# Kernel tuning notes

Hardware: AMD Instinct MI355X
Metric: run time of the kernel (lower is better)

Reference implementation:

```python
import jax, jax.numpy as jnp
import numpy as np

B, S, D, H = 1, 2048, 2048, 16
HD = D // H  # head_dim = 128
EPS = 1e-6


def setup_inputs() -> dict:
    key = jax.random.key(0)
    ks = jax.random.split(key, 12)
    sc = 0.02
    x = jax.random.normal(ks[0], (B, S, D), jnp.float32)
    wq = jax.random.normal(ks[1], (D, D), jnp.float32) * sc
    bq = jnp.zeros((D,), jnp.float32)
    wk = jax.random.normal(ks[2], (D, D), jnp.float32) * sc
    bk = jnp.zeros((D,), jnp.float32)
    wv = jax.random.normal(ks[3], (D, D), jnp.float32) * sc
    bv = jnp.zeros((D,), jnp.float32)
    wo = jax.random.normal(ks[4], (D, D), jnp.float32) * sc
    bo = jnp.zeros((D,), jnp.float32)
    gq = jnp.ones((D,), jnp.float32)  # RMSNorm weight for q
    gk = jnp.ones((D,), jnp.float32)  # RMSNorm weight for k
    # Rotary frequency table: complex freqs = cos + i*sin, shape [S, 1, HD//2]
    pos = jnp.arange(S, dtype=jnp.float32)
    inv = 1.0 / (10000.0 ** (jnp.arange(0, HD, 2, dtype=jnp.float32) / HD))  # [HD//2]
    theta = pos[:, None] * inv[None, :]  # [S, HD//2]
    freqs_cos = jnp.cos(theta)[:, None, :]  # [S, 1, HD//2]
    freqs_sin = jnp.sin(theta)[:, None, :]
    return {"x": x, "wq": wq, "bq": bq, "wk": wk, "bk": bk, "wv": wv, "bv": bv,
            "wo": wo, "bo": bo, "gq": gq, "gk": gk,
            "freqs_cos": freqs_cos, "freqs_sin": freqs_sin}


def _rmsnorm(x, g):
    # RMSNorm over full model dim (applied BEFORE head split, as in source)
    return x * jax.lax.rsqrt(jnp.mean(x * x, axis=-1, keepdims=True) + EPS) * g


def _rope(x, cos, sin):
    # x: [B,S,D] -> (B,S,H,HD//2,2) complex pairs; complex mult by (cos + i sin)
    b, s, d = x.shape
    xr = x.reshape(b, s, H, HD // 2, 2)
    a, bb = xr[..., 0], xr[..., 1]
    # cos/sin [S,1,HD//2] broadcast against [B,S,H,HD//2]
    ra = a * cos - bb * sin
    rb = a * sin + bb * cos
    return jnp.stack([ra, rb], axis=-1).reshape(b, s, d)


def reference(x, wq, bq, wk, bk, wv, bv, wo, bo, gq, gk, freqs_cos, freqs_sin):
    b, s, d = x.shape
    q = _rope(_rmsnorm(x @ wq.T + bq, gq), freqs_cos, freqs_sin)
    k = _rope(_rmsnorm(x @ wk.T + bk, gk), freqs_cos, freqs_sin)
    v = x @ wv.T + bv
    qh = q.reshape(b, s, H, HD).transpose(0, 2, 1, 3)  # [B,H,S,HD]
    kh = k.reshape(b, s, H, HD).transpose(0, 2, 1, 3)
    vh = v.reshape(b, s, H, HD).transpose(0, 2, 1, 3)
    scores = jnp.einsum('bhqd,bhkd->bhqk', qh, kh) / np.sqrt(HD).astype(np.float32)
    attn = jax.nn.softmax(scores, axis=-1)
    out = jnp.einsum('bhqk,bhkd->bhqd', attn, vh)
    out = out.transpose(0, 2, 1, 3).reshape(b, s, d)
    return out @ wo.T + bo
```

## Files before the change

### kernel.cpp

```cpp
#include <hip/hip_runtime.h>
#include <math.h>

typedef unsigned short u16;
typedef unsigned int u32;
typedef __bf16 bf16x8 __attribute__((ext_vector_type(8)));
typedef float f32x4 __attribute__((ext_vector_type(4)));
typedef float f32x16 __attribute__((ext_vector_type(16)));

__device__ __forceinline__ u16 f2bf(float f) {
  unsigned u = __float_as_uint(f);
  u += 0x7fff + ((u >> 16) & 1);
  return (u16)(u >> 16);
}

__device__ __forceinline__ u32 cvtpk(float lo, float hi) {
  u32 r;
  asm("v_cvt_pk_bf16_f32 %0, %1, %2" : "=v"(r) : "v"(lo), "v"(hi));
  return r;
}

__device__ __forceinline__ void pswap(u32& x, u32& y) {
  asm volatile("v_permlane32_swap_b32 %0, %1" : "+v"(x), "+v"(y));
}

__device__ __forceinline__ void gload_lds16(const void* g, void* l) {
  __builtin_amdgcn_global_load_lds(
      (const __attribute__((address_space(1))) unsigned int*)g,
      (__attribute__((address_space(3))) unsigned int*)l, 16, 0, 0);
}

__global__ __launch_bounds__(256) void k_cvt5(const float* __restrict__ s0,
                                              const float* __restrict__ s1,
                                              const float* __restrict__ s2,
                                              const float* __restrict__ s3,
                                              const float* __restrict__ s4,
                                              u16* __restrict__ dx,
                                              u16* __restrict__ dqkv,
                                              u16* __restrict__ dwo) {
  const int y = blockIdx.y;
  const float* s = (y == 0) ? s0 : (y == 1) ? s1 : (y == 2) ? s2
                   : (y == 3) ? s3 : s4;
  u16* d = (y == 0) ? dx : (y == 4) ? dwo : dqkv + (size_t)(y - 1) * 4194304;
  int i = (blockIdx.x * 256 + threadIdx.x) * 4;
  float4 v = *(const float4*)(s + i);
  ushort4 o;
  o.x = f2bf(v.x); o.y = f2bf(v.y); o.z = f2bf(v.z); o.w = f2bf(v.w);
  *(ushort4*)(d + i) = o;
}

__global__ __launch_bounds__(512, 4) void k_gemm_big(const u16* __restrict__ A,
                                                     const u16* __restrict__ B,
                                                     float* __restrict__ C,
                                                     int M, int N, int K) {
  __shared__ __align__(16) char lds[2][40960];
  const int tid = threadIdx.x;
  const int wid = tid >> 6, lane = tid & 63;
  const int lr = lane & 15, lg = lane >> 4;
  const int wm = (wid >> 2) * 64, wn = (wid & 3) * 48;
  const int nbx = N / 192, nby = M >> 7;
  const int colsPerXcd = nbx >> 3;
  const int xcd = blockIdx.x & 7, idx = blockIdx.x >> 3;
  const int bx = xcd * colsPerXcd + idx / nby;
  const int by = idx % nby;
  const int bm = by * 128, bn = bx * 192;
  const int srow = tid >> 3;
  const int schunk = (tid & 7) ^ (srow & 7);
  const size_t rsK = (size_t)K * 2;
  const char* gA = (const char*)A + (size_t)(bm + srow) * rsK + schunk * 16;
  const char* gB = (const char*)B + (size_t)(bn + srow) * rsK + schunk * 16;
  char* dA = (char*)lds + wid * 1024;
  char* dB = (char*)lds + 16384 + wid * 1024;

#define STAGE(cur, k0)                                                         \
  {                                                                            \
    _Pragma("unroll") for (int i = 0; i < 2; ++i)                              \
        gload_lds16(gA + (size_t)(i * 64) * rsK + (size_t)(k0) * 2,            \
                    dA + (cur) * 40960 + i * 8192);                            \
    _Pragma("unroll") for (int i = 0; i < 3; ++i)                              \
        gload_lds16(gB + (size_t)(i * 64) * rsK + (size_t)(k0) * 2,            \
                    dB + (cur) * 40960 + i * 8192);                            \
  }

  f32x4 acc[4][3] = {};
  STAGE(0, 0);
  STAGE(1, 64);
  asm volatile("s_waitcnt vmcnt(5)" ::: "memory");
  __builtin_amdgcn_s_barrier();
  const int NT = K >> 6;
  int cur = 0;
  const int rsw = (lr & 7);
  for (int t = 0; t < NT; ++t) {
    const char* La = (const char*)lds + cur * 40960;
    const char* Lb = La + 16384;
    bf16x8 af[4][2], bfr[3][2];
#pragma unroll
    for (int mi = 0; mi < 4; ++mi)
#pragma unroll
      for (int kk = 0; kk < 2; ++kk)
        af[mi][kk] = *(const bf16x8*)(La + (wm + mi * 16 + lr) * 128 +
                                      (((kk * 4 + lg) ^ rsw) * 16));
#pragma unroll
    for (int ni = 0; ni < 3; ++ni)
#pragma unroll
      for (int kk = 0; kk < 2; ++kk)
        bfr[ni][kk] = *(const bf16x8*)(Lb + (wn + ni * 16 + lr) * 128 +
                                       (((kk * 4 + lg) ^ rsw) * 16));
    asm volatile("s_waitcnt lgkmcnt(0)" ::: "memory");
    __builtin_amdgcn_s_barrier();
    if (t + 2 < NT) STAGE(cur, (t + 2) << 6);
    __builtin_amdgcn_s_setprio(1);
#pragma unroll
    for (int kk = 0; kk < 2; ++kk)
#pragma unroll
      for (int mi = 0; mi < 4; ++mi)
#pragma unroll
        for (int ni = 0; ni < 3; ++ni)
          acc[mi][ni] = __builtin_amdgcn_mfma_f32_16x16x32_bf16(
              af[mi][kk], bfr[ni][kk], acc[mi][ni], 0, 0, 0);
    __builtin_amdgcn_s_setprio(0);
    if (t + 2 < NT)
      asm volatile("s_waitcnt vmcnt(5)" ::: "memory");
    else
      asm volatile("s_waitcnt vmcnt(0)" ::: "memory");
    __builtin_amdgcn_s_barrier();
    cur ^= 1;
  }
#undef STAGE
#pragma unroll
  for (int mi = 0; mi < 4; ++mi)
#pragma unroll
    for (int ni = 0; ni < 3; ++ni)
#pragma unroll
      for (int j = 0; j < 4; ++j)
        C[(size_t)(bm + wm + mi * 16 + lg * 4 + j) * N + bn + wn + ni * 16 + lr] =
            acc[mi][ni][j];
}

__global__ __launch_bounds__(256, 2) void k_gemm_pipe(const u16* __restrict__ A,
                                                      const u16* __restrict__ B,
                                                      const float* __restrict__ bias,
                                                      float* __restrict__ C,
                                                      int M, int N, int K) {
  __shared__ __align__(16) char lds[2][24576];
  const int tid = threadIdx.x;
  const int wid = tid >> 6, lane = tid & 63;
  const int lr = lane & 15, lg = lane >> 4;
  const int wm = (wid >> 1) * 64, wn = (wid & 1) * 32;
  const int nbx = N >> 6, nby = M >> 7;
  const int colsPerXcd = nbx >> 3;
  const int xcd = blockIdx.x & 7, idx = blockIdx.x >> 3;
  const int bx = xcd * colsPerXcd + idx / nby;
  const int by = idx % nby;
  const int bm = by * 128, bn = bx * 64;
  const int srow = tid >> 3;
  const int schunk = (tid & 7) ^ (srow & 7);
  const size_t rsK = (size_t)K * 2;
  const char* gA = (const char*)A + (size_t)(bm + srow) * rsK + schunk * 16;
  const char* gB = (const char*)B + (size_t)(bn + srow) * rsK + schunk * 16;
  char* dA = (char*)lds + wid * 1024;
  char* dB = (char*)lds + 16384 + wid * 1024;

#define STAGE(cur, k0)                                                         \
  {                                                                            \
    _Pragma("unroll") for (int i = 0; i < 4; ++i)                              \
        gload_lds16(gA + (size_t)(i * 32) * rsK + (size_t)(k0) * 2,            \
                    dA + (cur) * 24576 + i * 4096);                            \
    _Pragma("unroll") for (int i = 0; i < 2; ++i)                              \
        gload_lds16(gB + (size_t)(i * 32) * rsK + (size_t)(k0) * 2,            \
                    dB + (cur) * 24576 + i * 4096);                            \
  }

  f32x4 acc[4][2] = {};
  STAGE(0, 0);
  STAGE(1, 64);
  asm volatile("s_waitcnt vmcnt(6)" ::: "memory");
  __builtin_amdgcn_s_barrier();
  const int NT = K >> 6;
  int cur = 0;
  const int rsw = (lr & 7);
  for (int t = 0; t < NT; ++t) {
    const char* La = (const char*)lds + cur * 24576;
    const char* Lb = La + 16384;
    bf16x8 af[4][2], bfr[2][2];
#pragma unroll
    for (int mi = 0; mi < 4; ++mi)
#pragma unroll
      for (int kk = 0; kk < 2; ++kk)
        af[mi][kk] = *(const bf16x8*)(La + (wm + mi * 16 + lr) * 128 +
                                      (((kk * 4 + lg) ^ rsw) * 16));
#pragma unroll
    for (int ni = 0; ni < 2; ++ni)
#pragma unroll
      for (int kk = 0; kk < 2; ++kk)
        bfr[ni][kk] = *(const bf16x8*)(Lb + (wn + ni * 16 + lr) * 128 +
                                       (((kk * 4 + lg) ^ rsw) * 16));
    asm volatile("s_waitcnt lgkmcnt(0)" ::: "memory");
    __builtin_amdgcn_s_barrier();
    if (t + 2 < NT) STAGE(cur, (t + 2) << 6);
    __builtin_amdgcn_s_setprio(1);
#pragma unroll
    for (int kk = 0; kk < 2; ++kk)
#pragma unroll
      for (int mi = 0; mi < 4; ++mi)
#pragma unroll
        for (int ni = 0; ni < 2; ++ni)
          acc[mi][ni] = __builtin_amdgcn_mfma_f32_16x16x32_bf16(
              af[mi][kk], bfr[ni][kk], acc[mi][ni], 0, 0, 0);
    __builtin_amdgcn_s_setprio(0);
    if (t + 2 < NT)
      asm volatile("s_waitcnt vmcnt(6)" ::: "memory");
    else
      asm volatile("s_waitcnt vmcnt(0)" ::: "memory");
    __builtin_amdgcn_s_barrier();
    cur ^= 1;
  }
#undef STAGE
#pragma unroll
  for (int mi = 0; mi < 4; ++mi)
#pragma unroll
    for (int ni = 0; ni < 2; ++ni) {
      int col = bn + wn + ni * 16 + lr;
      float bb = bias[col];
#pragma unroll
      for (int j = 0; j < 4; ++j)
        C[(size_t)(bm + wm + mi * 16 + lg * 4 + j) * N + col] =
            acc[mi][ni][j] + bb;
    }
}

__global__ __launch_bounds__(256) void k_rmsnorm_rope(
    const float* __restrict__ qkv, const float* __restrict__ bq,
    const float* __restrict__ bk, const float* __restrict__ gq,
    const float* __restrict__ gk, const float* __restrict__ fcos,
    const float* __restrict__ fsin, u16* __restrict__ qb, u16* __restrict__ kb) {
  const int s = blockIdx.x, which = blockIdx.y;
  const int t = threadIdx.x;
  const float* src = qkv + (size_t)s * 6144 + which * 2048;
  const float* bias = which ? bk : bq;
  const float* g = which ? gk : gq;
  u16* dst = (which ? kb : qb) + (size_t)s * 2048;
  const int c0 = t * 8;
  float4 a0 = *(const float4*)(src + c0);
  float4 a1 = *(const float4*)(src + c0 + 4);
  float4 b0 = *(const float4*)(bias + c0);
  float4 b1 = *(const float4*)(bias + c0 + 4);
  float v[8];
  v[0] = a0.x + b0.x; v[1] = a0.y + b0.y; v[2] = a0.z + b0.z; v[3] = a0.w + b0.w;
  v[4] = a1.x + b1.x; v[5] = a1.y + b1.y; v[6] = a1.z + b1.z; v[7] = a1.w + b1.w;
  float ss = 0.f;
#pragma unroll
  for (int j = 0; j < 8; ++j) ss += v[j] * v[j];
#pragma unroll
  for (int m = 1; m < 64; m <<= 1) ss += __shfl_xor(ss, m);
  __shared__ float red[4];
  if ((t & 63) == 0) red[t >> 6] = ss;
  __syncthreads();
  float r = rsqrtf((red[0] + red[1] + red[2] + red[3]) * (1.0f / 2048.0f) + 1e-6f);
  if (!which) r *= 0.08838834764831843f * 1.4426950408889634f;
  float4 g0 = *(const float4*)(g + c0);
  float4 g1 = *(const float4*)(g + c0 + 4);
  float gg[8] = {g0.x, g0.y, g0.z, g0.w, g1.x, g1.y, g1.z, g1.w};
  const int p0 = (c0 & 127) >> 1;
  u16 o[8];
#pragma unroll
  for (int j = 0; j < 4; ++j) {
    float a = v[2 * j] * r * gg[2 * j];
    float b = v[2 * j + 1] * r * gg[2 * j + 1];
    float co = fcos[s * 64 + p0 + j], si = fsin[s * 64 + p0 + j];
    o[2 * j]     = f2bf(a * co - b * si);
    o[2 * j + 1] = f2bf(a * si + b * co);
  }
  ushort4 q0; q0.x = o[0]; q0.y = o[1]; q0.z = o[2]; q0.w = o[3];
  ushort4 q1; q1.x = o[4]; q1.y = o[5]; q1.z = o[6]; q1.w = o[7];
  *(ushort4*)(dst + c0) = q0;
  *(ushort4*)(dst + c0 + 4) = q1;
}

__global__ __launch_bounds__(256) void k_transpose_v(const float* __restrict__ qkv,
                                                     const float* __restrict__ bv,
                                                     u16* __restrict__ vT) {
  __shared__ float tile[64][65];
  const int s0 = blockIdx.x * 64, d0 = blockIdx.y * 64;
  const int t = threadIdx.x;
  const int tc = (t & 15) * 4, tr = t >> 4;
  float4 bb = *(const float4*)(bv + d0 + tc);
#pragma unroll
  for (int i = 0; i < 4; ++i) {
    int sr = tr + i * 16;
    float4 x = *(const float4*)(qkv + (size_t)(s0 + sr) * 6144 + 4096 + d0 + tc);
    tile[sr][tc + 0] = x.x + bb.x;
    tile[sr][tc + 1] = x.y + bb.y;
    tile[sr][tc + 2] = x.z + bb.z;
    tile[sr][tc + 3] = x.w + bb.w;
  }
  __syncthreads();
#pragma unroll
  for (int i = 0; i < 4; ++i) {
    int dr = tr + i * 16;
    ushort4 o;
    o.x = f2bf(tile[tc + 0][dr]);
    o.y = f2bf(tile[tc + 1][dr]);
    o.z = f2bf(tile[tc + 2][dr]);
    o.w = f2bf(tile[tc + 3][dr]);
    *(ushort4*)(vT + (size_t)(d0 + dr) * 2048 + s0 + tc) = o;
  }
}

__global__ __launch_bounds__(256, 2) void k_attn(const u16* __restrict__ qb,
                                                 const u16* __restrict__ kb,
                                                 const u16* __restrict__ vT,
                                                 float* __restrict__ opart,
                                                 float* __restrict__ ml) {
  __shared__ __align__(16) char Ks[2][16384];
  __shared__ __align__(16) char Vs[2][16384];
  const int qt = blockIdx.x, h = blockIdx.y, ks = blockIdx.z;
  const int tid = threadIdx.x;
  const int wid = tid >> 6, lane = tid & 63;
  const int l31 = lane & 31, hi = lane >> 5;
  const int q0w = qt * 128 + wid * 32;
  const char* kbB = (const char*)kb;
  const char* vTB = (const char*)vT;
  const int krow = tid >> 4;
  const int kc = (tid & 15) ^ krow;
  const int vrow = tid >> 3;
  const int vc = (tid & 7) ^ (vrow & 7);

#define STAGE(buf, k0)                                                         \
  {                                                                            \
    _Pragma("unroll") for (int i = 0; i < 4; ++i)                              \
        gload_lds16(kbB + (size_t)((k0) + i * 16 + krow) * 4096 + h * 256 +    \
                        kc * 16,                                               \
                    (char*)Ks + (buf) * 16384 + i * 4096 + wid * 1024);        \
    _Pragma("unroll") for (int i = 0; i < 4; ++i)                              \
        gload_lds16(vTB + (size_t)(h * 128 + i * 32 + vrow) * 4096 +           \
                        (size_t)(k0) * 2 + vc * 16,                            \
                    (char*)Vs + (buf) * 16384 + i * 4096 + wid * 1024);        \
  }

  bf16x8 qf[8];
#pragma unroll
  for (int ds = 0; ds < 8; ++ds)
    qf[ds] = *(const bf16x8*)(qb + (size_t)(q0w + l31) * 2048 + h * 128 +
                              ds * 16 + hi * 8);
  f32x16 o[4] = {};
  float mrun = -3.0e38f, lsum = 0.f;
  const int kbeg = ks * 1024;
  const int ksw = l31 & 15, vsw = l31 & 7;
  STAGE(0, kbeg);
  __syncthreads();
  int cur = 0;
  for (int t = 0; t < 16; ++t) {
    if (t + 1 < 16) STAGE(cur ^ 1, kbeg + (t + 1) * 64);
    const char* Kc = Ks[cur];
    const char* Vc = Vs[cur];
    f32x16 p0 = {}, p1 = {};
    __builtin_amdgcn_s_setprio(1);
#pragma unroll
    for (int ds = 0; ds < 8; ++ds) {
      bf16x8 kf0 = *(const bf16x8*)(Kc + l31 * 256 + (((ds * 2 + hi) ^ ksw) * 16));
      p0 = __builtin_amdgcn_mfma_f32_32x32x16_bf16(kf0, qf[ds], p0, 0, 0, 0);
      bf16x8 kf1 = *(const bf16x8*)(Kc + (32 + l31) * 256 +
                                    (((ds * 2 + hi) ^ ksw) * 16));
      p1 = __builtin_amdgcn_mfma_f32_32x32x16_bf16(kf1, qf[ds], p1, 0, 0, 0);
    }
    __builtin_amdgcn_s_setprio(0);
    float pm = p0[0];
#pragma unroll
    for (int r = 1; r < 16; ++r) pm = fmaxf(pm, p0[r]);
#pragma unroll
    for (int r = 0; r < 16; ++r) pm = fmaxf(pm, p1[r]);
    pm = fmaxf(pm, __shfl_xor(pm, 32));
    if (!__all(pm <= mrun + 8.0f)) {
      float nm = fmaxf(mrun, pm);
      float fv = __builtin_amdgcn_exp2f(mrun - nm);
#pragma unroll
      for (int dt = 0; dt < 4; ++dt) o[dt] *= fv;
      lsum *= fv;
      mrun = nm;
    }
    float ls = 0.f;
#pragma unroll
    for (int r = 0; r < 16; ++r) { p0[r] = __builtin_amdgcn_exp2f(p0[r] - mrun); ls += p0[r]; }
#pragma unroll
    for (int r = 0; r < 16; ++r) { p1[r] = __builtin_amdgcn_exp2f(p1[r] - mrun); ls += p1[r]; }
    ls += __shfl_xor(ls, 32);
    lsum += ls;
    bf16x8 pa[4];
#pragma unroll
    for (int sl = 0; sl < 2; ++sl) {
      u32 E0 = cvtpk(p0[8 * sl + 0], p0[8 * sl + 1]);
      u32 E1 = cvtpk(p0[8 * sl + 2], p0[8 * sl + 3]);
      u32 O0 = cvtpk(p0[8 * sl + 4], p0[8 * sl + 5]);
      u32 O1 = cvtpk(p0[8 * sl + 6], p0[8 * sl + 7]);
      pswap(E0, O0); pswap(E1, O1);
      union { u32 w[4]; bf16x8 v; } uu;
      uu.w[0] = E0; uu.w[1] = E1; uu.w[2] = O0; uu.w[3] = O1;
      pa[sl] = uu.v;
    }
#pragma unroll
    for (int sl = 0; sl < 2; ++sl) {
      u32 E0 = cvtpk(p1[8 * sl + 0], p1[8 * sl + 1]);
      u32 E1 = cvtpk(p1[8 * sl + 2], p1[8 * sl + 3]);
      u32 O0 = cvtpk(p1[8 * sl + 4], p1[8 * sl + 5]);
      u32 O1 = cvtpk(p1[8 * sl + 6], p1[8 * sl + 7]);
      pswap(E0, O0); pswap(E1, O1);
      union { u32 w[4]; bf16x8 v; } uu;
      uu.w[0] = E0; uu.w[1] = E1; uu.w[2] = O0; uu.w[3] = O1;
      pa[2 + sl] = uu.v;
    }
    __builtin_amdgcn_s_setprio(1);
#pragma unroll
    for (int s = 0; s < 4; ++s)
#pragma unroll
      for (int dt = 0; dt < 4; ++dt) {
        bf16x8 vf = *(const bf16x8*)(Vc + (dt * 32 + l31) * 128 +
                                     (((s * 2 + hi) ^ vsw) * 16));
        o[dt] = __builtin_amdgcn_mfma_f32_32x32x16_bf16(pa[s], vf, o[dt], 0, 0, 0);
      }
    __builtin_amdgcn_s_setprio(0);
    __syncthreads();
    cur ^= 1;
  }
#undef STAGE
  float* opb = opart + ((size_t)ks * 32768 + (size_t)h * 2048 + q0w) * 128 + l31;
#pragma unroll
  for (int dt = 0; dt < 4; ++dt)
#pragma unroll
    for (int r = 0; r < 16; ++r)
      opb[(size_t)((r & 3) + 8 * (r >> 2) + 4 * hi) * 128 + dt * 32] = o[dt][r];
  if (lane < 32) {
    float2 v2; v2.x = mrun; v2.y = lsum;
    *(float2*)(ml + ((size_t)ks * 32768 + (size_t)h * 2048 + q0w + l31) * 2) = v2;
  }
}

__global__ __launch_bounds__(256) void k_attn_merge(const float* __restrict__ opart,
                                                    const float* __restrict__ ml,
                                                    u16* __restrict__ ob) {
  const int r = blockIdx.x * 8 + (threadIdx.x >> 5);
  const int d0 = (threadIdx.x & 31) * 4;
  float2 ml0 = *(const float2*)(ml + (size_t)r * 2);
  float2 ml1 = *(const float2*)(ml + (size_t)(32768 + r) * 2);
  float M = fmaxf(ml0.x, ml1.x);
  float f0 = __builtin_amdgcn_exp2f(ml0.x - M);
  float f1 = __builtin_amdgcn_exp2f(ml1.x - M);
  float inv = 1.0f / (ml0.y * f0 + ml1.y * f1);
  float4 a = *(const float4*)(opart + (size_t)r * 128 + d0);
  float4 b = *(const float4*)(opart + (size_t)(32768 + r) * 128 + d0);
  int h = r >> 11, q = r & 2047;
  ushort4 o;
  o.x = f2bf((a.x * f0 + b.x * f1) * inv);
  o.y = f2bf((a.y * f0 + b.y * f1) * inv);
  o.z = f2bf((a.z * f0 + b.z * f1) * inv);
  o.w = f2bf((a.w * f0 + b.w * f1) * inv);
  *(ushort4*)(ob + (size_t)q * 2048 + h * 128 + d0) = o;
}

extern "C" void kernel_launch(void* const* d_in, const int* in_sizes, int n_in,
                              void* d_out, int out_size, void* d_ws, size_t ws_size,
                              hipStream_t stream) {
  const float* x    = (const float*)d_in[0];
  const float* wq   = (const float*)d_in[1];
  const float* bq   = (const float*)d_in[2];
  const float* wk   = (const float*)d_in[3];
  const float* bk   = (const float*)d_in[4];
  const float* wv   = (const float*)d_in[5];
  const float* bv   = (const float*)d_in[6];
  const float* wo   = (const float*)d_in[7];
  const float* bo   = (const float*)d_in[8];
  const float* gq   = (const float*)d_in[9];
  const float* gk   = (const float*)d_in[10];
  const float* fcos = (const float*)d_in[11];
  const float* fsin = (const float*)d_in[12];

  char* ws = (char*)d_ws;
  float* qkv_pre = (float*)ws;
  float* opart = (float*)ws;
  float* ml    = (float*)(ws + 33554432);
  u16* xb   = (u16*)(ws + 50331648);
  u16* wqkv = (u16*)(ws + 58720256);
  u16* qb   = (u16*)(ws + 50331648);
  u16* kb   = (u16*)(ws + 58720256);
  u16* vT   = (u16*)(ws + 67108864);
  u16* ao   = (u16*)(ws + 75497472);
  u16* wob  = (u16*)(ws + 83886080);

  k_cvt5<<<dim3(4096, 5), 256, 0, stream>>>(x, wq, wk, wv, wo, xb, wqkv, wob);

  k_gemm_big<<<512, 512, 0, stream>>>(xb, wqkv, qkv_pre, 2048, 6144, 2048);
  k_rmsnorm_rope<<<dim3(2048, 2), 256, 0, stream>>>(qkv_pre, bq, bk, gq, gk,
                                                    fcos, fsin, qb, kb);
  k_transpose_v<<<dim3(32, 32), 256, 0, stream>>>(qkv_pre, bv, vT);
  k_attn<<<dim3(16, 16, 2), 256, 0, stream>>>(qb, kb, vT, opart, ml);
  k_attn_merge<<<4096, 256, 0, stream>>>(opart, ml, ao);
  k_gemm_pipe<<<dim3(512), 256, 0, stream>>>(ao, wob, bo, (float*)d_out,
                                             2048, 2048, 2048);
}
```

Before: 159.1 us.

## Single-buffer V in attention, raise occupancy, remap blocks per XCD

```diff
diff --git a/kernel.cpp b/kernel.cpp
--- a/kernel.cpp
+++ b/kernel.cpp
@@ -306,14 +306,18 @@
   }
 }
 
-__global__ __launch_bounds__(256, 2) void k_attn(const u16* __restrict__ qb,
+__global__ __launch_bounds__(256, 3) void k_attn(const u16* __restrict__ qb,
                                                  const u16* __restrict__ kb,
                                                  const u16* __restrict__ vT,
                                                  float* __restrict__ opart,
                                                  float* __restrict__ ml) {
   __shared__ __align__(16) char Ks[2][16384];
-  __shared__ __align__(16) char Vs[2][16384];
-  const int qt = blockIdx.x, h = blockIdx.y, ks = blockIdx.z;
+  __shared__ __align__(16) char Vs[16384];
+  const int bid = blockIdx.x;
+  const int xcd = bid & 7, j = bid >> 3;
+  const int h = xcd * 2 + (j & 1);
+  const int qt = (j >> 1) & 15;
+  const int ks = j >> 5;
   const int tid = threadIdx.x;
   const int wid = tid >> 6, lane = tid & 63;
   const int l31 = lane & 31, hi = lane >> 5;
@@ -325,16 +329,19 @@
   const int vrow = tid >> 3;
   const int vc = (tid & 7) ^ (vrow & 7);
 
-#define STAGE(buf, k0)                                                         \
+#define STAGE_K(buf, k0)                                                       \
   {                                                                            \
     _Pragma("unroll") for (int i = 0; i < 4; ++i)                              \
         gload_lds16(kbB + (size_t)((k0) + i * 16 + krow) * 4096 + h * 256 +    \
                         kc * 16,                                               \
                     (char*)Ks + (buf) * 16384 + i * 4096 + wid * 1024);        \
+  }
+#define STAGE_V(k0)                                                            \
+  {                                                                            \
     _Pragma("unroll") for (int i = 0; i < 4; ++i)                              \
         gload_lds16(vTB + (size_t)(h * 128 + i * 32 + vrow) * 4096 +           \
                         (size_t)(k0) * 2 + vc * 16,                            \
-                    (char*)Vs + (buf) * 16384 + i * 4096 + wid * 1024);        \
+                    (char*)Vs + i * 4096 + wid * 1024);                        \
   }
 
   bf16x8 qf[8];
@@ -346,13 +353,19 @@
   float mrun = -3.0e38f, lsum = 0.f;
   const int kbeg = ks * 1024;
   const int ksw = l31 & 15, vsw = l31 & 7;
-  STAGE(0, kbeg);
-  __syncthreads();
+  STAGE_K(0, kbeg);
   int cur = 0;
   for (int t = 0; t < 16; ++t) {
-    if (t + 1 < 16) STAGE(cur ^ 1, kbeg + (t + 1) * 64);
+    __builtin_amdgcn_s_barrier();
+    STAGE_V(kbeg + t * 64);
+    if (t < 15) {
+      STAGE_K(cur ^ 1, kbeg + (t + 1) * 64);
+      asm volatile("s_waitcnt vmcnt(8)" ::: "memory");
+    } else {
+      asm volatile("s_waitcnt vmcnt(4)" ::: "memory");
+    }
+    __builtin_amdgcn_s_barrier();
     const char* Kc = Ks[cur];
-    const char* Vc = Vs[cur];
     f32x16 p0 = {}, p1 = {};
     __builtin_amdgcn_s_setprio(1);
 #pragma unroll
@@ -364,27 +377,41 @@
       p1 = __builtin_amdgcn_mfma_f32_32x32x16_bf16(kf1, qf[ds], p1, 0, 0, 0);
     }
     __builtin_amdgcn_s_setprio(0);
-    float pm = p0[0];
-#pragma unroll
-    for (int r = 1; r < 16; ++r) pm = fmaxf(pm, p0[r]);
-#pragma unroll
-    for (int r = 0; r < 16; ++r) pm = fmaxf(pm, p1[r]);
-    pm = fmaxf(pm, __shfl_xor(pm, 32));
-    if (!__all(pm <= mrun + 8.0f)) {
-      float nm = fmaxf(mrun, pm);
-      float fv = __builtin_amdgcn_exp2f(mrun - nm);
-#pragma unroll
-      for (int dt = 0; dt < 4; ++dt) o[dt] *= fv;
-      lsum *= fv;
-      mrun = nm;
-    }
-    float ls = 0.f;
-#pragma unroll
-    for (int r = 0; r < 16; ++r) { p0[r] = __builtin_amdgcn_exp2f(p0[r] - mrun); ls += p0[r]; }
-#pragma unroll
-    for (int r = 0; r < 16; ++r) { p1[r] = __builtin_amdgcn_exp2f(p1[r] - mrun); ls += p1[r]; }
-    ls += __shfl_xor(ls, 32);
-    lsum += ls;
+    {
+      float tm[8];
+#pragma unroll
+      for (int r = 0; r < 8; ++r)
+        tm[r] = fmaxf(fmaxf(p0[2 * r], p0[2 * r + 1]),
+                      fmaxf(p1[2 * r], p1[2 * r + 1]));
+#pragma unroll
+      for (int s = 4; s > 0; s >>= 1)
+#pragma unroll
+        for (int r = 0; r < s; ++r) tm[r] = fmaxf(tm[r], tm[r + s]);
+      float pm = fmaxf(tm[0], __shfl_xor(tm[0], 32));
+      if (!__all(pm <= mrun + 8.0f)) {
+        float nm = fmaxf(mrun, pm);
+        float fv = __builtin_amdgcn_exp2f(mrun - nm);
+#pragma unroll
+        for (int dt = 0; dt < 4; ++dt) o[dt] *= fv;
+        lsum *= fv;
+        mrun = nm;
+      }
+    }
+    {
+#pragma unroll
+      for (int r = 0; r < 16; ++r) p0[r] = __builtin_amdgcn_exp2f(p0[r] - mrun);
+#pragma unroll
+      for (int r = 0; r < 16; ++r) p1[r] = __builtin_amdgcn_exp2f(p1[r] - mrun);
+      float ts[8];
+#pragma unroll
+      for (int r = 0; r < 8; ++r)
+        ts[r] = (p0[2 * r] + p0[2 * r + 1]) + (p1[2 * r] + p1[2 * r + 1]);
+#pragma unroll
+      for (int s = 4; s > 0; s >>= 1)
+#pragma unroll
+        for (int r = 0; r < s; ++r) ts[r] += ts[r + s];
+      lsum += ts[0] + __shfl_xor(ts[0], 32);
+    }
     bf16x8 pa[4];
 #pragma unroll
     for (int sl = 0; sl < 2; ++sl) {
@@ -408,20 +435,25 @@
       uu.w[0] = E0; uu.w[1] = E1; uu.w[2] = O0; uu.w[3] = O1;
       pa[2 + sl] = uu.v;
     }
+    if (t < 15)
+      asm volatile("s_waitcnt vmcnt(4)" ::: "memory");
+    else
+      asm volatile("s_waitcnt vmcnt(0)" ::: "memory");
+    __builtin_amdgcn_s_barrier();
     __builtin_amdgcn_s_setprio(1);
 #pragma unroll
     for (int s = 0; s < 4; ++s)
 #pragma unroll
       for (int dt = 0; dt < 4; ++dt) {
-        bf16x8 vf = *(const bf16x8*)(Vc + (dt * 32 + l31) * 128 +
+        bf16x8 vf = *(const bf16x8*)((const char*)Vs + (dt * 32 + l31) * 128 +
                                      (((s * 2 + hi) ^ vsw) * 16));
         o[dt] = __builtin_amdgcn_mfma_f32_32x32x16_bf16(pa[s], vf, o[dt], 0, 0, 0);
       }
     __builtin_amdgcn_s_setprio(0);
-    __syncthreads();
     cur ^= 1;
   }
-#undef STAGE
+#undef STAGE_K
+#undef STAGE_V
   float* opb = opart + ((size_t)ks * 32768 + (size_t)h * 2048 + q0w) * 128 + l31;
 #pragma unroll
   for (int dt = 0; dt < 4; ++dt)
@@ -491,7 +523,7 @@
   k_rmsnorm_rope<<<dim3(2048, 2), 256, 0, stream>>>(qkv_pre, bq, bk, gq, gk,
                                                     fcos, fsin, qb, kb);
   k_transpose_v<<<dim3(32, 32), 256, 0, stream>>>(qkv_pre, bv, vT);
-  k_attn<<<dim3(16, 16, 2), 256, 0, stream>>>(qb, kb, vT, opart, ml);
+  k_attn<<<512, 256, 0, stream>>>(qb, kb, vT, opart, ml);
   k_attn_merge<<<4096, 256, 0, stream>>>(opart, ml, ao);
   k_gemm_pipe<<<dim3(512), 256, 0, stream>>>(ao, wob, bo, (float*)d_out,
                                              2048, 2048, 2048);
```

After: 170.5 us. 7.1% more time.

## Software-pipeline attention loop and remap blocks to XCDs by head

Applied to the files above, without the earlier changes.

```diff
diff --git a/kernel.cpp b/kernel.cpp
--- a/kernel.cpp
+++ b/kernel.cpp
@@ -313,7 +313,11 @@
                                                  float* __restrict__ ml) {
   __shared__ __align__(16) char Ks[2][16384];
   __shared__ __align__(16) char Vs[2][16384];
-  const int qt = blockIdx.x, h = blockIdx.y, ks = blockIdx.z;
+  const int bid = blockIdx.x;
+  const int xcd = bid & 7, j = bid >> 3;
+  const int h = xcd * 2 + (j & 1);
+  const int qt = (j >> 1) & 15;
+  const int ks = j >> 5;
   const int tid = threadIdx.x;
   const int wid = tid >> 6, lane = tid & 63;
   const int l31 = lane & 31, hi = lane >> 5;
@@ -325,16 +329,94 @@
   const int vrow = tid >> 3;
   const int vc = (tid & 7) ^ (vrow & 7);
 
-#define STAGE(buf, k0)                                                         \
+#define STAGE_K(buf, k0)                                                       \
   {                                                                            \
     _Pragma("unroll") for (int i = 0; i < 4; ++i)                              \
         gload_lds16(kbB + (size_t)((k0) + i * 16 + krow) * 4096 + h * 256 +    \
                         kc * 16,                                               \
                     (char*)Ks + (buf) * 16384 + i * 4096 + wid * 1024);        \
+  }
+#define STAGE_V(buf, k0)                                                       \
+  {                                                                            \
     _Pragma("unroll") for (int i = 0; i < 4; ++i)                              \
         gload_lds16(vTB + (size_t)(h * 128 + i * 32 + vrow) * 4096 +           \
                         (size_t)(k0) * 2 + vc * 16,                            \
                     (char*)Vs + (buf) * 16384 + i * 4096 + wid * 1024);        \
+  }
+
+#define QK_TILE(KBUF, P0, P1)                                                  \
+  {                                                                            \
+    __builtin_amdgcn_s_setprio(1);                                             \
+    _Pragma("unroll") for (int ds = 0; ds < 8; ++ds) {                         \
+      bf16x8 kf0 = *(const bf16x8*)((KBUF) + l31 * 256 +                       \
+                                    (((ds * 2 + hi) ^ ksw) * 16));             \
+      P0 = __builtin_amdgcn_mfma_f32_32x32x16_bf16(kf0, qf[ds], P0, 0, 0, 0);  \
+      bf16x8 kf1 = *(const bf16x8*)((KBUF) + (32 + l31) * 256 +                \
+                                    (((ds * 2 + hi) ^ ksw) * 16));             \
+      P1 = __builtin_amdgcn_mfma_f32_32x32x16_bf16(kf1, qf[ds], P1, 0, 0, 0);  \
+    }                                                                          \
+    __builtin_amdgcn_s_setprio(0);                                             \
+  }
+
+#define SOFTMAX_CVT(P0, P1, PA)                                                \
+  {                                                                            \
+    float tm[8];                                                               \
+    _Pragma("unroll") for (int r = 0; r < 8; ++r)                              \
+        tm[r] = fmaxf(fmaxf(P0[2 * r], P0[2 * r + 1]),                         \
+                      fmaxf(P1[2 * r], P1[2 * r + 1]));                        \
+    _Pragma("unroll") for (int s = 4; s > 0; s >>= 1)                          \
+        _Pragma("unroll") for (int r = 0; r < s; ++r)                          \
+            tm[r] = fmaxf(tm[r], tm[r + s]);                                   \
+    float pm = fmaxf(tm[0], __shfl_xor(tm[0], 32));                            \
+    if (!__all(pm <= mrun + 8.0f)) {                                           \
+      float nm = fmaxf(mrun, pm);                                              \
+      float fv = __builtin_amdgcn_exp2f(mrun - nm);                            \
+      _Pragma("unroll") for (int dt = 0; dt < 4; ++dt) o[dt] *= fv;            \
+      lsum *= fv;                                                              \
+      mrun = nm;                                                               \
+    }                                                                          \
+    _Pragma("unroll") for (int r = 0; r < 16; ++r)                             \
+        P0[r] = __builtin_amdgcn_exp2f(P0[r] - mrun);                          \
+    _Pragma("unroll") for (int r = 0; r < 16; ++r)                             \
+        P1[r] = __builtin_amdgcn_exp2f(P1[r] - mrun);                          \
+    float ts[8];                                                               \
+    _Pragma("unroll") for (int r = 0; r < 8; ++r)                              \
+        ts[r] = (P0[2 * r] + P0[2 * r + 1]) + (P1[2 * r] + P1[2 * r + 1]);     \
+    _Pragma("unroll") for (int s = 4; s > 0; s >>= 1)                          \
+        _Pragma("unroll") for (int r = 0; r < s; ++r) ts[r] += ts[r + s];      \
+    lsum += ts[0] + __shfl_xor(ts[0], 32);                                     \
+    _Pragma("unroll") for (int sl = 0; sl < 2; ++sl) {                         \
+      u32 E0 = cvtpk(P0[8 * sl + 0], P0[8 * sl + 1]);                          \
+      u32 E1 = cvtpk(P0[8 * sl + 2], P0[8 * sl + 3]);                          \
+      u32 O0 = cvtpk(P0[8 * sl + 4], P0[8 * sl + 5]);                          \
+      u32 O1 = cvtpk(P0[8 * sl + 6], P0[8 * sl + 7]);                          \
+      pswap(E0, O0); pswap(E1, O1);                                            \
+      union { u32 w[4]; bf16x8 v; } uu;                                        \
+      uu.w[0] = E0; uu.w[1] = E1; uu.w[2] = O0; uu.w[3] = O1;                  \
+      PA[sl] = uu.v;                                                           \
+    }                                                                          \
+    _Pragma("unroll") for (int sl = 0; sl < 2; ++sl) {                         \
+      u32 E0 = cvtpk(P1[8 * sl + 0], P1[8 * sl + 1]);                          \
+      u32 E1 = cvtpk(P1[8 * sl + 2], P1[8 * sl + 3]);                          \
+      u32 O0 = cvtpk(P1[8 * sl + 4], P1[8 * sl + 5]);                          \
+      u32 O1 = cvtpk(P1[8 * sl + 6], P1[8 * sl + 7]);                          \
+      pswap(E0, O0); pswap(E1, O1);                                            \
+      union { u32 w[4]; bf16x8 v; } uu;                                        \
+      uu.w[0] = E0; uu.w[1] = E1; uu.w[2] = O0; uu.w[3] = O1;                  \
+      PA[2 + sl] = uu.v;                                                       \
+    }                                                                          \
+  }
+
+#define PV_TILE(VBUF, PA)                                                      \
+  {                                                                            \
+    __builtin_amdgcn_s_setprio(1);                                             \
+    _Pragma("unroll") for (int s = 0; s < 4; ++s)                              \
+        _Pragma("unroll") for (int dt = 0; dt < 4; ++dt) {                     \
+      bf16x8 vf = *(const bf16x8*)((VBUF) + (dt * 32 + l31) * 128 +            \
+                                   (((s * 2 + hi) ^ vsw) * 16));               \
+      o[dt] = __builtin_amdgcn_mfma_f32_32x32x16_bf16(PA[s], vf, o[dt], 0,0,0);\
+    }                                                                          \
+    __builtin_amdgcn_s_setprio(0);                                             \
   }
 
   bf16x8 qf[8];
@@ -346,82 +428,42 @@
   float mrun = -3.0e38f, lsum = 0.f;
   const int kbeg = ks * 1024;
   const int ksw = l31 & 15, vsw = l31 & 7;
-  STAGE(0, kbeg);
+  const f32x16 zero = {};
+  bf16x8 pa[4];
+
+  STAGE_K(0, kbeg);
+  STAGE_K(1, kbeg + 64);
+  STAGE_V(0, kbeg);
+  STAGE_V(1, kbeg + 64);
+  asm volatile("s_waitcnt vmcnt(0)" ::: "memory");
+  __builtin_amdgcn_s_barrier();
+  f32x16 pA0 = {}, pA1 = {}, pB0 = {}, pB1 = {};
+  QK_TILE(Ks[0], pA0, pA1);
   __syncthreads();
-  int cur = 0;
-  for (int t = 0; t < 16; ++t) {
-    if (t + 1 < 16) STAGE(cur ^ 1, kbeg + (t + 1) * 64);
-    const char* Kc = Ks[cur];
-    const char* Vc = Vs[cur];
-    f32x16 p0 = {}, p1 = {};
-    __builtin_amdgcn_s_setprio(1);
-#pragma unroll
-    for (int ds = 0; ds < 8; ++ds) {
-      bf16x8 kf0 = *(const bf16x8*)(Kc + l31 * 256 + (((ds * 2 + hi) ^ ksw) * 16));
-      p0 = __builtin_amdgcn_mfma_f32_32x32x16_bf16(kf0, qf[ds], p0, 0, 0, 0);
-      bf16x8 kf1 = *(const bf16x8*)(Kc + (32 + l31) * 256 +
-                                    (((ds * 2 + hi) ^ ksw) * 16));
-      p1 = __builtin_amdgcn_mfma_f32_32x32x16_bf16(kf1, qf[ds], p1, 0, 0, 0);
-    }
-    __builtin_amdgcn_s_setprio(0);
-    float pm = p0[0];
-#pragma unroll
-    for (int r = 1; r < 16; ++r) pm = fmaxf(pm, p0[r]);
-#pragma unroll
-    for (int r = 0; r < 16; ++r) pm = fmaxf(pm, p1[r]);
-    pm = fmaxf(pm, __shfl_xor(pm, 32));
-    if (!__all(pm <= mrun + 8.0f)) {
-      float nm = fmaxf(mrun, pm);
-      float fv = __builtin_amdgcn_exp2f(mrun - nm);
-#pragma unroll
-      for (int dt = 0; dt < 4; ++dt) o[dt] *= fv;
-      lsum *= fv;
-      mrun = nm;
-    }
-    float ls = 0.f;
-#pragma unroll
-    for (int r = 0; r < 16; ++r) { p0[r] = __builtin_amdgcn_exp2f(p0[r] - mrun); ls += p0[r]; }
-#pragma unroll
-    for (int r = 0; r < 16; ++r) { p1[r] = __builtin_amdgcn_exp2f(p1[r] - mrun); ls += p1[r]; }
-    ls += __shfl_xor(ls, 32);
-    lsum += ls;
-    bf16x8 pa[4];
-#pragma unroll
-    for (int sl = 0; sl < 2; ++sl) {
-      u32 E0 = cvtpk(p0[8 * sl + 0], p0[8 * sl + 1]);
-      u32 E1 = cvtpk(p0[8 * sl + 2], p0[8 * sl + 3]);
-      u32 O0 = cvtpk(p0[8 * sl + 4], p0[8 * sl + 5]);
-      u32 O1 = cvtpk(p0[8 * sl + 6], p0[8 * sl + 7]);
-      pswap(E0, O0); pswap(E1, O1);
-      union { u32 w[4]; bf16x8 v; } uu;
-      uu.w[0] = E0; uu.w[1] = E1; uu.w[2] = O0; uu.w[3] = O1;
-      pa[sl] = uu.v;
-    }
-#pragma unroll
-    for (int sl = 0; sl < 2; ++sl) {
-      u32 E0 = cvtpk(p1[8 * sl + 0], p1[8 * sl + 1]);
-      u32 E1 = cvtpk(p1[8 * sl + 2], p1[8 * sl + 3]);
-      u32 O0 = cvtpk(p1[8 * sl + 4], p1[8 * sl + 5]);
-      u32 O1 = cvtpk(p1[8 * sl + 6], p1[8 * sl + 7]);
-      pswap(E0, O0); pswap(E1, O1);
-      union { u32 w[4]; bf16x8 v; } uu;
-      uu.w[0] = E0; uu.w[1] = E1; uu.w[2] = O0; uu.w[3] = O1;
-      pa[2 + sl] = uu.v;
-    }
-    __builtin_amdgcn_s_setprio(1);
-#pragma unroll
-    for (int s = 0; s < 4; ++s)
-#pragma unroll
-      for (int dt = 0; dt < 4; ++dt) {
-        bf16x8 vf = *(const bf16x8*)(Vc + (dt * 32 + l31) * 128 +
-                                     (((s * 2 + hi) ^ vsw) * 16));
-        o[dt] = __builtin_amdgcn_mfma_f32_32x32x16_bf16(pa[s], vf, o[dt], 0, 0, 0);
-      }
-    __builtin_amdgcn_s_setprio(0);
-    __syncthreads();
-    cur ^= 1;
-  }
-#undef STAGE
+
+  for (int t = 0; t < 16; t += 2) {
+    pB0 = zero; pB1 = zero;
+    QK_TILE(Ks[1], pB0, pB1);
+    if (t < 14) STAGE_K(0, kbeg + (t + 2) * 64);
+    SOFTMAX_CVT(pA0, pA1, pa);
+    PV_TILE(Vs[0], pa);
+    asm volatile("s_waitcnt vmcnt(0) lgkmcnt(0)" ::: "memory");
+    __builtin_amdgcn_s_barrier();
+    if (t < 14) STAGE_V(0, kbeg + (t + 2) * 64);
+    pA0 = zero; pA1 = zero;
+    if (t < 14) QK_TILE(Ks[0], pA0, pA1);
+    if (t < 13) STAGE_K(1, kbeg + (t + 3) * 64);
+    SOFTMAX_CVT(pB0, pB1, pa);
+    PV_TILE(Vs[1], pa);
+    asm volatile("s_waitcnt vmcnt(0) lgkmcnt(0)" ::: "memory");
+    __builtin_amdgcn_s_barrier();
+    if (t < 13) STAGE_V(1, kbeg + (t + 3) * 64);
+  }
+#undef STAGE_K
+#undef STAGE_V
+#undef QK_TILE
+#undef SOFTMAX_CVT
+#undef PV_TILE
   float* opb = opart + ((size_t)ks * 32768 + (size_t)h * 2048 + q0w) * 128 + l31;
 #pragma unroll
   for (int dt = 0; dt < 4; ++dt)
@@ -491,7 +533,7 @@
   k_rmsnorm_rope<<<dim3(2048, 2), 256, 0, stream>>>(qkv_pre, bq, bk, gq, gk,
                                                     fcos, fsin, qb, kb);
   k_transpose_v<<<dim3(32, 32), 256, 0, stream>>>(qkv_pre, bv, vT);
-  k_attn<<<dim3(16, 16, 2), 256, 0, stream>>>(qb, kb, vT, opart, ml);
+  k_attn<<<512, 256, 0, stream>>>(qb, kb, vT, opart, ml);
   k_attn_merge<<<4096, 256, 0, stream>>>(opart, ml, ao);
   k_gemm_pipe<<<dim3(512), 256, 0, stream>>>(ao, wob, bo, (float*)d_out,
                                              2048, 2048, 2048);
```

After: 158.4 us. Within noise of the previous version (-0.4%).
